# Kernel optimization log

Measured on AMD Instinct MI355X. Metric: run time of the kernel, lower is better.

Reference implementation:

```python
import jax, jax.numpy as jnp
import numpy as np
from jax import lax

B, C, H, W = 2, 256, 64, 64
CI = C // 2           # inter_channels = 128
CH = CI // 2          # key/query channels = 64
EPS = 1e-5


def conv1x1(x, w, b):
    # x: [B,C,H,W], w: [O,C], b: [O]
    return jnp.einsum('oc,bchw->bohw', w, x) + b[None, :, None, None]


def bn(x, g, be, m, v):
    inv = (g / jnp.sqrt(v + EPS))[None, :, None, None]
    return (x - m[None, :, None, None]) * inv + be[None, :, None, None]


def setup_inputs() -> dict:
    key = jax.random.key(0)
    ks = jax.random.split(key, 40)
    r = lambda i, shape, sc=0.05: jax.random.normal(ks[i], shape, dtype=jnp.float32) * sc
    u = lambda i, shape: jax.random.uniform(ks[i], shape, dtype=jnp.float32, minval=0.5, maxval=1.5)
    return {
        'q': jax.random.normal(ks[0], (B, C, H, W), dtype=jnp.float32),
        's': jax.random.normal(ks[1], (B, C, H, W), dtype=jnp.float32),
        'scale': jnp.full((1,), 0.3, dtype=jnp.float32),
        'w_v': r(2, (CI, C)), 'b_v': r(3, (CI,)),
        'w_k1': r(4, (CH, C)), 'b_k1': r(5, (CH,)),
        'w_q1': r(6, (CH, C)), 'b_q1': r(7, (CH,)),
        'w_k2': r(8, (CH, C)), 'b_k2': r(9, (CH,)),
        'w_q2': r(10, (CH, C)), 'b_q2': r(11, (CH,)),
        'w_ts': r(12, (CI, C)), 'b_ts': r(13, (CI,)),
        'g_ts': u(14, (CI,)), 'be_ts': r(15, (CI,)), 'm_ts': r(16, (CI,)), 'v_ts': u(17, (CI,)),
        'w_tq': r(18, (CI, C)), 'b_tq': r(19, (CI,)),
        'g_tq': u(20, (CI,)), 'be_tq': r(21, (CI,)), 'm_tq': r(22, (CI,)), 'v_tq': u(23, (CI,)),
        'w_cat': r(24, (CI, 2 * CI, 3, 3)),
        'g_cat': u(25, (CI,)), 'be_cat': r(26, (CI,)), 'm_cat': r(27, (CI,)), 'v_cat': u(28, (CI,)),
    }


def reference(q, s, scale, w_v, b_v, w_k1, b_k1, w_q1, b_q1, w_k2, b_k2, w_q2, b_q2,
              w_ts, b_ts, g_ts, be_ts, m_ts, v_ts,
              w_tq, b_tq, g_tq, be_tq, m_tq, v_tq,
              w_cat, g_cat, be_cat, m_cat, v_cat):
    b_, _, h, w = q.shape
    n = h * w
    # values: [B, N, CI]
    v_q = conv1x1(q, w_v, b_v).reshape(b_, CI, n).transpose(0, 2, 1)
    v_s = conv1x1(s, w_v, b_v).reshape(b_, CI, n).transpose(0, 2, 1)
    # concatenated keys/queries: [B, CI, N]
    k_x = jnp.concatenate([conv1x1(q, w_k1, b_k1), conv1x1(s, w_k2, b_k2)], axis=1).reshape(b_, CI, n)
    q_x = jnp.concatenate([conv1x1(q, w_q1, b_q1), conv1x1(s, w_q2, b_q2)], axis=1).reshape(b_, CI, n)
    # affinity: [B, N, N]
    A_s = jnp.einsum('bcn,bcm->bnm', k_x, q_x)
    attn_s = jax.nn.softmax(A_s, axis=-1)
    attn_q = jax.nn.softmax(jnp.transpose(A_s, (0, 2, 1)), axis=-1)
    # p_s: [B, N, CI] -> [B, CI, H, W]
    p_s = jnp.einsum('bnm,bmc->bnc', attn_s, v_s).transpose(0, 2, 1).reshape(b_, CI, h, w)
    s_t = bn(conv1x1(s, w_ts, b_ts), g_ts, be_ts, m_ts, v_ts)
    q_t = bn(conv1x1(q, w_tq, b_tq), g_tq, be_tq, m_tq, v_tq)
    E_s = scale[0] * p_s + s_t
    q_s_ = jnp.einsum('bnm,bmc->bnc', attn_q, v_q).transpose(0, 2, 1).reshape(b_, CI, h, w)
    E_q = scale[0] * q_s_ + q_t
    cat = jnp.concatenate([E_q, E_s], axis=1)
    conv = lax.conv_general_dilated(cat, w_cat, (1, 1), 'SAME',
                                    dimension_numbers=('NCHW', 'OIHW', 'NCHW'))
    cpam = jax.nn.relu(bn(conv, g_cat, be_cat, m_cat, v_cat))
    return (cpam, E_q, E_s)
```

## Files before the change

### kernel.cpp

```cpp
#include <hip/hip_runtime.h>
#include <hip/hip_bf16.h>

#define NPIX 4096
#define NCH  256
#define CI   128
#define EPS  1e-5f
#define SOFF 20.0f

typedef unsigned short u16;
typedef __attribute__((ext_vector_type(8))) short short8;
typedef __attribute__((ext_vector_type(4))) float f32x4;
typedef __attribute__((ext_vector_type(16))) float f32x16;

__device__ __forceinline__ float bfu2f(u16 u) {
    union { unsigned int i; float f; } x; x.i = ((unsigned int)u) << 16; return x.f;
}
__device__ __forceinline__ u16 f2bfu(float f) {
    union { float ff; unsigned int i; } x; x.ff = f;
    unsigned int r = x.i + 0x7FFFu + ((x.i >> 16) & 1u);
    return (u16)(r >> 16);
}

__device__ __forceinline__ void gload16(const u16* g, u16* l) {
    __builtin_amdgcn_global_load_lds(
        (const __attribute__((address_space(1))) unsigned int*)g,
        (__attribute__((address_space(3))) unsigned int*)l,
        16, 0, 0);
}

__global__ __launch_bounds__(256) void prep_kernel(
    const float* __restrict__ w_v,
    const float* __restrict__ w_k1, const float* __restrict__ w_q1,
    const float* __restrict__ w_k2, const float* __restrict__ w_q2,
    const float* __restrict__ w_ts, const float* __restrict__ w_tq,
    u16* __restrict__ Wbf,
    const float* __restrict__ w_cat, u16* __restrict__ wT)
{
    const int bx = blockIdx.x;
    if (bx < 768) {
        int idx = bx * 256 + threadIdx.x;
        int src = idx / 98304;
        int r   = idx - src * 98304;
        int o   = r >> 8, c = r & 255;
        float v;
        if (o < 128)      v = w_v[(size_t)o * 256 + c];
        else if (o < 192) v = (src ? w_k2 : w_k1)[(size_t)(o - 128) * 256 + c];
        else if (o < 256) v = (src ? w_q2 : w_q1)[(size_t)(o - 192) * 256 + c];
        else              v = (src ? w_ts : w_tq)[(size_t)(o - 256) * 256 + c];
        Wbf[idx] = f2bfu(v);
    } else {
        int co = bx - 768;
        const float* srcb = w_cat + (size_t)co * 2304;
        u16* dstb = wT + (size_t)co * 2304;
        for (int t = threadIdx.x; t < 2304; t += 256) {
            int ic = t / 9, tap = t - ic * 9;
            dstb[tap * 256 + ic] = f2bfu(srcb[t]);
        }
    }
}

__global__ __launch_bounds__(256) void proj2_kernel(
    const float* __restrict__ xq, const float* __restrict__ xs,
    const u16* __restrict__ Wbf,
    const float* __restrict__ b_v,
    const float* __restrict__ b_k1, const float* __restrict__ b_q1,
    const float* __restrict__ b_k2, const float* __restrict__ b_q2,
    const float* __restrict__ b_ts, const float* __restrict__ g_ts,
    const float* __restrict__ be_ts, const float* __restrict__ m_ts,
    const float* __restrict__ v_ts,
    const float* __restrict__ b_tq, const float* __restrict__ g_tq,
    const float* __restrict__ be_tq, const float* __restrict__ m_tq,
    const float* __restrict__ v_tq,
    u16* __restrict__ kT, u16* __restrict__ qT,
    u16* __restrict__ vq, u16* __restrict__ vs,
    u16* __restrict__ tq, u16* __restrict__ ts)
{
    __shared__ u16 Xs[64 * 264];
    __shared__ u16 KQ[64 * 136];

    const int tid  = threadIdx.x;
    const int lane = tid & 63;
    const int wid  = tid >> 6;
    const int l16  = lane & 15;
    const int quad = lane >> 4;

    const int n0  = blockIdx.x * 64;
    const int bz  = blockIdx.z;
    const int b   = bz >> 1, src = bz & 1;

    const float* xg = (src ? xs : xq) + (size_t)b * NCH * NPIX + n0;
    #pragma unroll
    for (int k0 = 0; k0 < 64; k0 += 16) {
        float v[16];
        #pragma unroll
        for (int k = 0; k < 16; ++k) {
            int idx = tid + (k0 + k) * 256;
            int c = idx >> 6, n = idx & 63;
            v[k] = xg[(size_t)c * NPIX + n];
        }
        #pragma unroll
        for (int k = 0; k < 16; ++k) {
            int idx = tid + (k0 + k) * 256;
            int c = idx >> 6, n = idx & 63;
            Xs[n * 264 + c] = f2bfu(v[k]);
        }
    }
    __syncthreads();

    const u16* W = Wbf + (size_t)src * 384 * 256;
    const int o0w = wid * 96;
    const float* bk = src ? b_k2 : b_k1;
    const float* bq = src ? b_q2 : b_q1;
    const float* bt = src ? b_ts : b_tq;

    f32x4 acc[24];
    #pragma unroll
    for (int ot = 0; ot < 6; ++ot) {
        int ob = o0w + ot * 16 + quad * 4;
        const float* bp;
        if (ob < 128)      bp = b_v + ob;
        else if (ob < 192) bp = bk + (ob - 128);
        else if (ob < 256) bp = bq + (ob - 192);
        else               bp = bt + (ob - 256);
        float4 b4 = *(const float4*)bp;
        f32x4 iv = (f32x4){b4.x, b4.y, b4.z, b4.w};
        #pragma unroll
        for (int pt = 0; pt < 4; ++pt) acc[ot * 4 + pt] = iv;
    }

    #pragma unroll
    for (int kc = 0; kc < 8; ++kc) {
        short8 bfr[4];
        #pragma unroll
        for (int pt = 0; pt < 4; ++pt)
            bfr[pt] = *(const short8*)&Xs[(pt * 16 + l16) * 264 + kc * 32 + quad * 8];
        #pragma unroll
        for (int ot = 0; ot < 6; ++ot) {
            short8 a = *(const short8*)&W[(size_t)(o0w + ot * 16 + l16) * 256 + kc * 32 + quad * 8];
            #pragma unroll
            for (int pt = 0; pt < 4; ++pt)
                acc[ot * 4 + pt] = __builtin_amdgcn_mfma_f32_16x16x32_bf16(a, bfr[pt], acc[ot * 4 + pt], 0, 0, 0);
        }
    }

    #pragma unroll
    for (int ot = 0; ot < 6; ++ot) {
        int ob = o0w + ot * 16;
        #pragma unroll
        for (int pt = 0; pt < 4; ++pt) {
            int px = pt * 16 + l16;
            f32x4 v4 = acc[ot * 4 + pt];
            if (ob < 128) {
                u16* dst = src ? vs : vq;
                #pragma unroll
                for (int r = 0; r < 4; ++r)
                    dst[((size_t)b * CI + ob + quad * 4 + r) * NPIX + n0 + px] = f2bfu(v4[r]);
            } else if (ob < 256) {
                int colb = (ob < 192) ? (ob - 128) : (64 + ob - 192);
                #pragma unroll
                for (int r = 0; r < 4; ++r)
                    KQ[px * 136 + colb + quad * 4 + r] = f2bfu(v4[r]);
            } else {
                const float* g  = src ? g_ts  : g_tq;
                const float* be = src ? be_ts : be_tq;
                const float* mm = src ? m_ts  : m_tq;
                const float* vv = src ? v_ts  : v_tq;
                u16* dst = src ? ts : tq;
                #pragma unroll
                for (int r = 0; r < 4; ++r) {
                    int oc = ob - 256 + quad * 4 + r;
                    float inv = g[oc] * rsqrtf(vv[oc] + EPS);
                    dst[((size_t)b * CI + oc) * NPIX + n0 + px] =
                        f2bfu((v4[r] - mm[oc]) * inv + be[oc]);
                }
            }
        }
    }
    __syncthreads();

    const int chb = src ? 64 : 0;
    #pragma unroll
    for (int u = 0; u < 4; ++u) {
        int idx = tid + u * 256;
        int px = idx >> 4, oct = idx & 15;
        uint4 val = *(const uint4*)&KQ[px * 136 + oct * 8];
        if (oct < 8)
            *(uint4*)&kT[((size_t)b * NPIX + n0 + px) * CI + chb + oct * 8] = val;
        else
            *(uint4*)&qT[((size_t)b * NPIX + n0 + px) * CI + chb + (oct - 8) * 8] = val;
    }
}

#define AKS_OFF 0
#define AVT_OFF 8192
#define ASMEM_U16 16384

__global__ __launch_bounds__(128) void attn_kernel(
    const u16* __restrict__ kT, const u16* __restrict__ qT,
    const u16* __restrict__ vq, const u16* __restrict__ vs,
    u16* __restrict__ Opart, float* __restrict__ Lpart, int nseg)
{
    __shared__ __align__(16) u16 smem[ASMEM_U16];

    const int tid  = threadIdx.x;
    const int lane = tid & 63;
    const int qh   = tid >> 6;
    const int l32  = lane & 31;
    const int h    = lane >> 5;

    const int nt = blockIdx.x;
    const int n0 = nt * 64;
    const int at = blockIdx.y;
    const int z  = blockIdx.z;
    const int b  = z / nseg;
    const int seg = z - b * nseg;

    const u16* Qg = at ? qT : kT;
    const u16* Kg = at ? kT : qT;
    const u16* Vg = at ? vq : vs;

    short8 qf[8];
    {
        const u16* Qb = Qg + ((size_t)b * NPIX + n0 + qh * 32 + l32) * CI;
        #pragma unroll
        for (int kc = 0; kc < 8; ++kc)
            qf[kc] = *(const short8*)&Qb[kc * 16 + h * 8];
    }

    f32x16 o[4];
    #pragma unroll
    for (int ct = 0; ct < 4; ++ct)
        #pragma unroll
        for (int r = 0; r < 16; ++r) o[ct][r] = 0.f;
    float L = 0.f;

    const u16* KgB = Kg + (size_t)b * NPIX * CI;
    const u16* VgB = Vg + (size_t)b * CI * NPIX;

    const int mt0 = seg * (128 / nseg);
    const int mt1 = mt0 + (128 / nseg);

    const int fv = (l32 >> 1) & 3;

    #define ISSUE_TILE(buf, m0_)                                              \
    {                                                                         \
        u16* kb_ = smem + AKS_OFF + (buf) * 4096;                             \
        u16* vb_ = smem + AVT_OFF + (buf) * 4096;                             \
        _Pragma("unroll")                                                     \
        for (int k = 0; k < 4; ++k) {                                         \
            int sb  = k * 128 + qh * 64;                                      \
            int idx = sb + lane;                                              \
            int row = idx >> 4, p = idx & 15;                                 \
            int pg = p ^ (row & 15);                                          \
            gload16(KgB + (size_t)((m0_) + row) * CI + pg * 8, kb_ + sb * 8); \
        }                                                                     \
        _Pragma("unroll")                                                     \
        for (int k = 0; k < 4; ++k) {                                         \
            int sb  = k * 128 + qh * 64;                                      \
            int idx = sb + lane;                                              \
            int c = idx >> 2, p = idx & 3;                                    \
            int pg = p ^ ((c >> 1) & 3);                                      \
            gload16(VgB + (size_t)c * NPIX + (m0_) + pg * 8, vb_ + sb * 8);   \
        }                                                                     \
    }

    int cur = 0;
    ISSUE_TILE(0, mt0 * 32);

    for (int mt = mt0; mt < mt1; ++mt) {
        __syncthreads();
        if (mt + 1 < mt1) ISSUE_TILE(1 - cur, (mt + 1) * 32);

        const u16* Ks = smem + AKS_OFF + cur * 4096;
        const u16* Vt = smem + AVT_OFF + cur * 4096;

        f32x16 c;
        #pragma unroll
        for (int r = 0; r < 16; ++r) c[r] = 0.f;
        __builtin_amdgcn_s_setprio(1);
        #pragma unroll
        for (int kc = 0; kc < 8; ++kc) {
            short8 kf = *(const short8*)&Ks[l32 * 128 + (((kc * 2 + h) ^ (l32 & 15)) * 8)];
            c = __builtin_amdgcn_mfma_f32_32x32x16_bf16(kf, qf[kc], c, 0, 0, 0);
        }
        __builtin_amdgcn_s_setprio(0);

        unsigned int pk[8];
        float Lsum = 0.f;
        #pragma unroll
        for (int t = 0; t < 8; ++t) {
            float p0 = __expf(c[2 * t]     - SOFF);
            float p1 = __expf(c[2 * t + 1] - SOFF);
            Lsum += p0 + p1;
            asm("v_cvt_pk_bf16_f32 %0, %1, %2" : "=v"(pk[t]) : "v"(p0), "v"(p1));
        }
        Lsum += __shfl_xor(Lsum, 32);
        L += Lsum;

        unsigned int pw0 = __shfl_xor(pk[0], 32), pw1 = __shfl_xor(pk[1], 32);
        unsigned int pw2 = __shfl_xor(pk[2], 32), pw3 = __shfl_xor(pk[3], 32);
        unsigned int pw4 = __shfl_xor(pk[4], 32), pw5 = __shfl_xor(pk[5], 32);
        unsigned int pw6 = __shfl_xor(pk[6], 32), pw7 = __shfl_xor(pk[7], 32);
        union { unsigned int u[4]; short8 s8; } a0, a1;
        a0.u[0] = h ? pw2 : pk[0];
        a0.u[1] = h ? pw3 : pk[1];
        a0.u[2] = h ? pk[2] : pw0;
        a0.u[3] = h ? pk[3] : pw1;
        a1.u[0] = h ? pw6 : pk[4];
        a1.u[1] = h ? pw7 : pk[5];
        a1.u[2] = h ? pk[6] : pw4;
        a1.u[3] = h ? pk[7] : pw5;

        __builtin_amdgcn_s_setprio(1);
        #pragma unroll
        for (int ct = 0; ct < 4; ++ct) {
            int ci = ct * 32 + l32;
            short8 b0 = *(const short8*)&Vt[ci * 32 + (((    h) ^ fv) * 8)];
            o[ct] = __builtin_amdgcn_mfma_f32_32x32x16_bf16(a0.s8, b0, o[ct], 0, 0, 0);
            short8 b1 = *(const short8*)&Vt[ci * 32 + (((2 + h) ^ fv) * 8)];
            o[ct] = __builtin_amdgcn_mfma_f32_32x32x16_bf16(a1.s8, b1, o[ct], 0, 0, 0);
        }
        __builtin_amdgcn_s_setprio(0);
        cur ^= 1;
    }

    const size_t tile = (((size_t)(at * 2 + b) * 64 + nt) * nseg + seg);
    u16* Ob = Opart + tile * 8192;
    #pragma unroll
    for (int r = 0; r < 16; ++r) {
        int row = qh * 32 + (r & 3) + 8 * (r >> 2) + 4 * h;
        #pragma unroll
        for (int ct = 0; ct < 4; ++ct)
            Ob[row * 128 + ct * 32 + l32] = f2bfu(o[ct][r]);
    }
    if (h == 0)
        Lpart[tile * 64 + qh * 32 + l32] = L;
    #undef ISSUE_TILE
}

__global__ __launch_bounds__(256) void attn_combine_kernel(
    const u16* __restrict__ Opart, const float* __restrict__ Lpart,
    const u16* __restrict__ tq, const u16* __restrict__ ts,
    const float* __restrict__ scale_p,
    float* __restrict__ out, u16* __restrict__ Ebf, int nseg)
{
    __shared__ float Of[128 * 68];
    __shared__ float invL[64];

    const int tid = threadIdx.x;
    const int nt = blockIdx.x;
    const int n0 = nt * 64;
    const int at = blockIdx.y;
    const int b  = blockIdx.z;

    const u16* Tg = at ? tq : ts;
    float* outE   = out + (size_t)(at ? 1 : 2) * 1048576;
    const int ch0 = at ? 0 : 128;
    const size_t tbase = ((size_t)(at * 2 + b) * 64 + nt) * nseg;

    if (tid < 64) {
        float Lg = 0.f;
        for (int s = 0; s < nseg; ++s) Lg += Lpart[(tbase + s) * 64 + tid];
        invL[tid] = 1.f / Lg;
    }
    __syncthreads();

    #pragma unroll
    for (int k = 0; k < 4; ++k) {
        int idx = tid + k * 256;
        int row = idx >> 4, oct = idx & 15;
        float m[8] = {0.f, 0.f, 0.f, 0.f, 0.f, 0.f, 0.f, 0.f};
        for (int s = 0; s < nseg; ++s) {
            union { uint4 v; u16 u[8]; } pk;
            pk.v = *(const uint4*)&Opart[(tbase + s) * 8192 + row * 128 + oct * 8];
            #pragma unroll
            for (int j = 0; j < 8; ++j) m[j] += bfu2f(pk.u[j]);
        }
        float w = invL[row];
        #pragma unroll
        for (int j = 0; j < 8; ++j)
            Of[(oct * 8 + j) * 68 + row] = m[j] * w;
    }
    __syncthreads();

    float scale = *scale_p;
    const u16* Tb = Tg + (size_t)b * CI * NPIX + n0;
    float* Ob = outE + (size_t)b * CI * NPIX + n0;
    for (int idx = tid; idx < 128 * 64; idx += 256) {
        int c = idx >> 6, r = idx & 63;
        float v = scale * Of[c * 68 + r] + bfu2f(Tb[(size_t)c * NPIX + r]);
        Ob[(size_t)c * NPIX + r] = v;
        Ebf[((size_t)b * NPIX + n0 + r) * NCH + ch0 + c] = f2bfu(v);
    }
}

#define CXT_STR 40

__global__ __launch_bounds__(256) void conv_kernel(
    const u16* __restrict__ Ebf,
    const u16* __restrict__ wT,
    const float* __restrict__ g_cat, const float* __restrict__ be_cat,
    const float* __restrict__ m_cat, const float* __restrict__ v_cat,
    float* __restrict__ out)
{
    __shared__ u16 XtW[4][3 * 34 * CXT_STR];

    const int tid  = threadIdx.x;
    const int lane = tid & 63;
    const int wid  = tid >> 6;
    const int l16  = lane & 15;
    const int quad = lane >> 4;

    const int h    = blockIdx.x;
    const int coff = blockIdx.y * 32;
    const int b    = blockIdx.z;

    const int cot = wid >> 1;
    const int pxt = (wid & 1) * 2;
    const int gc0 = pxt * 16 - 1;

    f32x4 acc[2];
    #pragma unroll
    for (int j = 0; j < 2; ++j) acc[j] = (f32x4){0.f, 0.f, 0.f, 0.f};

    const u16* Eb = Ebf + (size_t)b * NPIX * NCH;
    u16* Xw = &XtW[wid][0];
    const int cobase = coff + cot * 16 + l16;

    for (int icc = 0; icc < 8; ++icc) {
        const int ic0 = icc * 32;

        short8 wfrag[9];
        #pragma unroll
        for (int tap = 0; tap < 9; ++tap)
            wfrag[tap] = *(const short8*)&wT[((size_t)cobase * 9 + tap) * 256 + ic0 + quad * 8];

        for (int u = lane; u < 408; u += 64) {
            int part = u & 3, xe = u >> 2;
            int dh = xe / 34, x = xe - dh * 34;
            int gr = h + dh - 1, gc = gc0 + x;
            uint4 val = make_uint4(0u, 0u, 0u, 0u);
            if ((unsigned)gr < 64u && (unsigned)gc < 64u)
                val = *(const uint4*)&Eb[((size_t)gr * 64 + gc) * NCH + ic0 + part * 8];
            *(uint4*)&Xw[(dh * 34 + x) * CXT_STR + part * 8] = val;
        }

        #pragma unroll
        for (int tap = 0; tap < 9; ++tap) {
            const int dh = tap / 3, dw = tap % 3;
            short8 bf[2];
            #pragma unroll
            for (int j = 0; j < 2; ++j) {
                int x = j * 16 + l16 + dw;
                bf[j] = *(const short8*)&Xw[(dh * 34 + x) * CXT_STR + quad * 8];
            }
            #pragma unroll
            for (int j = 0; j < 2; ++j)
                acc[j] = __builtin_amdgcn_mfma_f32_16x16x32_bf16(wfrag[tap], bf[j], acc[j], 0, 0, 0);
        }
    }

    #pragma unroll
    for (int r = 0; r < 4; ++r) {
        int co = coff + cot * 16 + quad * 4 + r;
        float inv = g_cat[co] * rsqrtf(v_cat[co] + EPS);
        float mm  = m_cat[co];
        float be  = be_cat[co];
        #pragma unroll
        for (int j = 0; j < 2; ++j) {
            int wcol = (pxt + j) * 16 + l16;
            float v = (acc[j][r] - mm) * inv + be;
            out[((size_t)b * CI + co) * NPIX + h * 64 + wcol] = fmaxf(v, 0.f);
        }
    }
}

extern "C" void kernel_launch(void* const* d_in, const int* in_sizes, int n_in,
                              void* d_out, int out_size, void* d_ws, size_t ws_size,
                              hipStream_t stream)
{
    const float* q     = (const float*)d_in[0];
    const float* s     = (const float*)d_in[1];
    const float* scale = (const float*)d_in[2];
    const float* w_v   = (const float*)d_in[3];
    const float* b_v   = (const float*)d_in[4];
    const float* w_k1  = (const float*)d_in[5];
    const float* b_k1  = (const float*)d_in[6];
    const float* w_q1  = (const float*)d_in[7];
    const float* b_q1  = (const float*)d_in[8];
    const float* w_k2  = (const float*)d_in[9];
    const float* b_k2  = (const float*)d_in[10];
    const float* w_q2  = (const float*)d_in[11];
    const float* b_q2  = (const float*)d_in[12];
    const float* w_ts  = (const float*)d_in[13];
    const float* b_ts  = (const float*)d_in[14];
    const float* g_ts  = (const float*)d_in[15];
    const float* be_ts = (const float*)d_in[16];
    const float* m_ts  = (const float*)d_in[17];
    const float* v_ts  = (const float*)d_in[18];
    const float* w_tq  = (const float*)d_in[19];
    const float* b_tq  = (const float*)d_in[20];
    const float* g_tq  = (const float*)d_in[21];
    const float* be_tq = (const float*)d_in[22];
    const float* m_tq  = (const float*)d_in[23];
    const float* v_tq  = (const float*)d_in[24];
    const float* w_cat = (const float*)d_in[25];
    const float* g_cat = (const float*)d_in[26];
    const float* be_cat= (const float*)d_in[27];
    const float* m_cat = (const float*)d_in[28];
    const float* v_cat = (const float*)d_in[29];

    float* out = (float*)d_out;
    u16* ws = (u16*)d_ws;
    const size_t SZ = (size_t)2 * CI * NPIX;
    u16* kT  = ws;
    u16* qT  = kT + SZ;
    u16* vq  = qT + SZ;
    u16* vs  = vq + SZ;
    u16* tq  = vs + SZ;
    u16* ts  = tq + SZ;
    u16* Wbf = ts + SZ;
    u16* B   = Wbf + 196608;
    u16* Ebf = B;
    u16* wTc = B + 2097152;
    u16* Opart = wTc + 294912;

    const size_t fixed_u16 = 6 * SZ + 196608 + 2097152 + 294912;
    int nseg = 1;
    {
        size_t need4 = (fixed_u16 + (size_t)4 * 2097152) * 2 + (size_t)4 * 131072;
        size_t need2 = (fixed_u16 + (size_t)2 * 2097152) * 2 + (size_t)2 * 131072;
        if (ws_size >= need4)      nseg = 4;
        else if (ws_size >= need2) nseg = 2;
    }
    float* Lpart = (float*)(Opart + (size_t)nseg * 256 * 8192);

    dim3 blk(256);
    hipLaunchKernelGGL(prep_kernel, dim3(896), blk, 0, stream,
                       w_v, w_k1, w_q1, w_k2, w_q2, w_ts, w_tq, Wbf, w_cat, wTc);
    hipLaunchKernelGGL(proj2_kernel, dim3(64, 1, 4), blk, 0, stream,
                       q, s, Wbf, b_v, b_k1, b_q1, b_k2, b_q2,
                       b_ts, g_ts, be_ts, m_ts, v_ts,
                       b_tq, g_tq, be_tq, m_tq, v_tq,
                       kT, qT, vq, vs, tq, ts);
    hipLaunchKernelGGL(attn_kernel, dim3(64, 2, 2 * nseg), dim3(128), 0, stream,
                       kT, qT, vq, vs, Opart, Lpart, nseg);
    hipLaunchKernelGGL(attn_combine_kernel, dim3(64, 2, 2), blk, 0, stream,
                       Opart, Lpart, tq, ts, scale, out, Ebf, nseg);
    hipLaunchKernelGGL(conv_kernel, dim3(64, 4, 2), blk, 0, stream,
                       Ebf, wTc, g_cat, be_cat, m_cat, v_cat, out);
}
```

Baseline: 245.4 us.

## Load attention K fragments directly to registers and use permlane32 swaps

```diff
diff --git a/kernel.cpp b/kernel.cpp
--- a/kernel.cpp
+++ b/kernel.cpp
@@ -191,9 +191,7 @@
     }
 }
 
-#define AKS_OFF 0
-#define AVT_OFF 8192
-#define ASMEM_U16 16384
+#define ASMEM_U16 8192
 
 __global__ __launch_bounds__(128) void attn_kernel(
     const u16* __restrict__ kT, const u16* __restrict__ qT,
@@ -242,87 +240,92 @@
 
     const int fv = (l32 >> 1) & 3;
 
-    #define ISSUE_TILE(buf, m0_)                                              \
+    const int pg = (tid & 3) ^ ((tid >> 3) & 3);
+    const u16* Vsrc = VgB + (size_t)(tid >> 2) * NPIX + pg * 8;
+
+    const u16* Kp = KgB + ((size_t)(mt0 * 32) + l32) * CI + h * 8;
+
+    short8 kfA[8], kfB[8];
+    #pragma unroll
+    for (int kc = 0; kc < 8; ++kc) kfA[kc] = *(const short8*)&Kp[kc * 16];
+
+    #define ISSUE_V(BUF2, M0_)                                                \
+    {   u16* vb_ = smem + (BUF2) * 4096;                                      \
+        _Pragma("unroll")                                                     \
+        for (int k = 0; k < 4; ++k)                                           \
+            gload16(Vsrc + (size_t)k * 32 * NPIX + (M0_),                     \
+                    vb_ + (k * 128 + qh * 64) * 8);                           \
+    }
+
+    ISSUE_V(0, mt0 * 32);
+
+    #define STEP(KFC, KFN, BUF, MT)                                           \
     {                                                                         \
-        u16* kb_ = smem + AKS_OFF + (buf) * 4096;                             \
-        u16* vb_ = smem + AVT_OFF + (buf) * 4096;                             \
+               \
+        f32x16 c;                                                             \
+        _Pragma("unroll") for (int r = 0; r < 16; ++r) c[r] = 0.f;            \
+        __builtin_amdgcn_s_setprio(1);                                        \
         _Pragma("unroll")                                                     \
-        for (int k = 0; k < 4; ++k) {                                         \
-            int sb  = k * 128 + qh * 64;                                      \
-            int idx = sb + lane;                                              \
-            int row = idx >> 4, p = idx & 15;                                 \
-            int pg = p ^ (row & 15);                                          \
-            gload16(KgB + (size_t)((m0_) + row) * CI + pg * 8, kb_ + sb * 8); \
+        for (int kc = 0; kc < 8; ++kc)                                        \
+            c = __builtin_amdgcn_mfma_f32_32x32x16_bf16(KFC[kc], qf[kc], c, 0, 0, 0); \
+        __builtin_amdgcn_s_setprio(0);                                        \
+               \
+        unsigned int pk[8];                                                   \
+        float Lsum = 0.f;                                                     \
+        _Pragma("unroll")                                                     \
+        for (int t = 0; t < 8; ++t) {                                         \
+            float p0 = __expf(c[2 * t]     - SOFF);                           \
+            float p1 = __expf(c[2 * t + 1] - SOFF);                           \
+            Lsum += p0 + p1;                                                  \
+            asm("v_cvt_pk_bf16_f32 %0, %1, %2" : "=v"(pk[t]) : "v"(p0), "v"(p1)); \
         }                                                                     \
+        {                                                                     \
+            union { float f; unsigned int u; } lu; lu.f = Lsum;               \
+            unsigned int la = lu.u, lb = lu.u;                                \
+            asm("v_permlane32_swap_b32 %0, %1" : "+v"(la), "+v"(lb));         \
+            union { unsigned int u; float f; } lp; lp.u = h ? la : lb;        \
+            L += Lsum + lp.f;                                                 \
+        }                                                                     \
+          \
+        unsigned int x0 = pk[0], x2 = pk[2];                                  \
+        asm("v_permlane32_swap_b32 %0, %1" : "+v"(x0), "+v"(x2));             \
+        unsigned int x1 = pk[1], x3 = pk[3];                                  \
+        asm("v_permlane32_swap_b32 %0, %1" : "+v"(x1), "+v"(x3));             \
+        unsigned int x4 = pk[4], x6 = pk[6];                                  \
+        asm("v_permlane32_swap_b32 %0, %1" : "+v"(x4), "+v"(x6));             \
+        unsigned int x5 = pk[5], x7 = pk[7];                                  \
+        asm("v_permlane32_swap_b32 %0, %1" : "+v"(x5), "+v"(x7));             \
+        union { unsigned int u[4]; short8 s8; } a0, a1;                       \
+        a0.u[0] = x0; a0.u[1] = x1; a0.u[2] = x2; a0.u[3] = x3;               \
+        a1.u[0] = x4; a1.u[1] = x5; a1.u[2] = x6; a1.u[3] = x7;               \
+        __syncthreads();           \
+        if ((MT) + 1 < mt1) {                                                 \
+            ISSUE_V(1 - (BUF), ((MT) + 1) * 32);                              \
+            Kp += 32 * CI;                                                    \
+            _Pragma("unroll")                                                 \
+            for (int kc = 0; kc < 8; ++kc)                                    \
+                KFN[kc] = *(const short8*)&Kp[kc * 16];                       \
+        }                                                                     \
+                  \
+        const u16* Vt = smem + (BUF) * 4096;                                  \
+        __builtin_amdgcn_s_setprio(1);                                        \
         _Pragma("unroll")                                                     \
-        for (int k = 0; k < 4; ++k) {                                         \
-            int sb  = k * 128 + qh * 64;                                      \
-            int idx = sb + lane;                                              \
-            int c = idx >> 2, p = idx & 3;                                    \
-            int pg = p ^ ((c >> 1) & 3);                                      \
-            gload16(VgB + (size_t)c * NPIX + (m0_) + pg * 8, vb_ + sb * 8);   \
+        for (int ct = 0; ct < 4; ++ct) {                                      \
+            int ci = ct * 32 + l32;                                           \
+            short8 b0 = *(const short8*)&Vt[ci * 32 + ((h ^ fv) * 8)];        \
+            o[ct] = __builtin_amdgcn_mfma_f32_32x32x16_bf16(a0.s8, b0, o[ct], 0, 0, 0); \
+            short8 b1 = *(const short8*)&Vt[ci * 32 + (((2 + h) ^ fv) * 8)];  \
+            o[ct] = __builtin_amdgcn_mfma_f32_32x32x16_bf16(a1.s8, b1, o[ct], 0, 0, 0); \
         }                                                                     \
-    }
-
-    int cur = 0;
-    ISSUE_TILE(0, mt0 * 32);
-
-    for (int mt = mt0; mt < mt1; ++mt) {
-        __syncthreads();
-        if (mt + 1 < mt1) ISSUE_TILE(1 - cur, (mt + 1) * 32);
-
-        const u16* Ks = smem + AKS_OFF + cur * 4096;
-        const u16* Vt = smem + AVT_OFF + cur * 4096;
-
-        f32x16 c;
-        #pragma unroll
-        for (int r = 0; r < 16; ++r) c[r] = 0.f;
-        __builtin_amdgcn_s_setprio(1);
-        #pragma unroll
-        for (int kc = 0; kc < 8; ++kc) {
-            short8 kf = *(const short8*)&Ks[l32 * 128 + (((kc * 2 + h) ^ (l32 & 15)) * 8)];
-            c = __builtin_amdgcn_mfma_f32_32x32x16_bf16(kf, qf[kc], c, 0, 0, 0);
-        }
-        __builtin_amdgcn_s_setprio(0);
-
-        unsigned int pk[8];
-        float Lsum = 0.f;
-        #pragma unroll
-        for (int t = 0; t < 8; ++t) {
-            float p0 = __expf(c[2 * t]     - SOFF);
-            float p1 = __expf(c[2 * t + 1] - SOFF);
-            Lsum += p0 + p1;
-            asm("v_cvt_pk_bf16_f32 %0, %1, %2" : "=v"(pk[t]) : "v"(p0), "v"(p1));
-        }
-        Lsum += __shfl_xor(Lsum, 32);
-        L += Lsum;
-
-        unsigned int pw0 = __shfl_xor(pk[0], 32), pw1 = __shfl_xor(pk[1], 32);
-        unsigned int pw2 = __shfl_xor(pk[2], 32), pw3 = __shfl_xor(pk[3], 32);
-        unsigned int pw4 = __shfl_xor(pk[4], 32), pw5 = __shfl_xor(pk[5], 32);
-        unsigned int pw6 = __shfl_xor(pk[6], 32), pw7 = __shfl_xor(pk[7], 32);
-        union { unsigned int u[4]; short8 s8; } a0, a1;
-        a0.u[0] = h ? pw2 : pk[0];
-        a0.u[1] = h ? pw3 : pk[1];
-        a0.u[2] = h ? pk[2] : pw0;
-        a0.u[3] = h ? pk[3] : pw1;
-        a1.u[0] = h ? pw6 : pk[4];
-        a1.u[1] = h ? pw7 : pk[5];
-        a1.u[2] = h ? pk[6] : pw4;
-        a1.u[3] = h ? pk[7] : pw5;
-
-        __builtin_amdgcn_s_setprio(1);
-        #pragma unroll
-        for (int ct = 0; ct < 4; ++ct) {
-            int ci = ct * 32 + l32;
-            short8 b0 = *(const short8*)&Vt[ci * 32 + (((    h) ^ fv) * 8)];
-            o[ct] = __builtin_amdgcn_mfma_f32_32x32x16_bf16(a0.s8, b0, o[ct], 0, 0, 0);
-            short8 b1 = *(const short8*)&Vt[ci * 32 + (((2 + h) ^ fv) * 8)];
-            o[ct] = __builtin_amdgcn_mfma_f32_32x32x16_bf16(a1.s8, b1, o[ct], 0, 0, 0);
-        }
-        __builtin_amdgcn_s_setprio(0);
-        cur ^= 1;
-    }
+        __builtin_amdgcn_s_setprio(0);                                        \
+    }
+
+    for (int mt = mt0; mt < mt1; mt += 2) {
+        STEP(kfA, kfB, 0, mt)
+        STEP(kfB, kfA, 1, mt + 1)
+    }
+    #undef STEP
+    #undef ISSUE_V
 
     const size_t tile = (((size_t)(at * 2 + b) * 64 + nt) * nseg + seg);
     u16* Ob = Opart + tile * 8192;
@@ -335,7 +338,6 @@
     }
     if (h == 0)
         Lpart[tile * 64 + qh * 32 + l32] = L;
-    #undef ISSUE_TILE
 }
 
 __global__ __launch_bounds__(256) void attn_combine_kernel(
```

After: 265.5 us. 1.08x slower.

## Load V fragments directly from global, use permlane32 swaps, allow eight key segments

Applied to the files above, without the earlier changes.

```diff
diff --git a/kernel.cpp b/kernel.cpp
--- a/kernel.cpp
+++ b/kernel.cpp
@@ -191,11 +191,9 @@
     }
 }
 
-#define AKS_OFF 0
-#define AVT_OFF 8192
-#define ASMEM_U16 16384
-
-__global__ __launch_bounds__(128) void attn_kernel(
+#define ASMEM_U16 8192
+
+__global__ __launch_bounds__(128, 3) void attn_kernel(
     const u16* __restrict__ kT, const u16* __restrict__ qT,
     const u16* __restrict__ vq, const u16* __restrict__ vs,
     u16* __restrict__ Opart, float* __restrict__ Lpart, int nseg)
@@ -237,15 +235,15 @@
     const u16* KgB = Kg + (size_t)b * NPIX * CI;
     const u16* VgB = Vg + (size_t)b * CI * NPIX;
 
-    const int mt0 = seg * (128 / nseg);
-    const int mt1 = mt0 + (128 / nseg);
-
-    const int fv = (l32 >> 1) & 3;
-
-    #define ISSUE_TILE(buf, m0_)                                              \
+    const int mtn = 128 / nseg;
+    const int mt0 = seg * mtn;
+    const int mt1 = mt0 + mtn;
+
+    const u16* Vb = VgB + (size_t)l32 * NPIX + h * 8;
+
+    #define ISSUE_K(buf, m0_)                                                 \
     {                                                                         \
-        u16* kb_ = smem + AKS_OFF + (buf) * 4096;                             \
-        u16* vb_ = smem + AVT_OFF + (buf) * 4096;                             \
+        u16* kb_ = smem + (buf) * 4096;                                       \
         _Pragma("unroll")                                                     \
         for (int k = 0; k < 4; ++k) {                                         \
             int sb  = k * 128 + qh * 64;                                      \
@@ -254,25 +252,26 @@
             int pg = p ^ (row & 15);                                          \
             gload16(KgB + (size_t)((m0_) + row) * CI + pg * 8, kb_ + sb * 8); \
         }                                                                     \
-        _Pragma("unroll")                                                     \
-        for (int k = 0; k < 4; ++k) {                                         \
-            int sb  = k * 128 + qh * 64;                                      \
-            int idx = sb + lane;                                              \
-            int c = idx >> 2, p = idx & 3;                                    \
-            int pg = p ^ ((c >> 1) & 3);                                      \
-            gload16(VgB + (size_t)c * NPIX + (m0_) + pg * 8, vb_ + sb * 8);   \
-        }                                                                     \
     }
 
     int cur = 0;
-    ISSUE_TILE(0, mt0 * 32);
+    ISSUE_K(0, mt0 * 32);
 
     for (int mt = mt0; mt < mt1; ++mt) {
+        const int m0 = mt * 32;
         __syncthreads();
-        if (mt + 1 < mt1) ISSUE_TILE(1 - cur, (mt + 1) * 32);
-
-        const u16* Ks = smem + AKS_OFF + cur * 4096;
-        const u16* Vt = smem + AVT_OFF + cur * 4096;
+
+        short8 vf[8];
+        #pragma unroll
+        for (int ct = 0; ct < 4; ++ct) {
+            vf[2 * ct]     = *(const short8*)&Vb[(size_t)(ct * 32) * NPIX + m0];
+            vf[2 * ct + 1] = *(const short8*)&Vb[(size_t)(ct * 32) * NPIX + m0 + 16];
+        }
+        __builtin_amdgcn_sched_barrier(0);
+
+        if (mt + 1 < mt1) ISSUE_K(1 - cur, (mt + 1) * 32);
+
+        const u16* Ks = smem + cur * 4096;
 
         f32x16 c;
         #pragma unroll
@@ -294,35 +293,36 @@
             Lsum += p0 + p1;
             asm("v_cvt_pk_bf16_f32 %0, %1, %2" : "=v"(pk[t]) : "v"(p0), "v"(p1));
         }
-        Lsum += __shfl_xor(Lsum, 32);
-        L += Lsum;
-
-        unsigned int pw0 = __shfl_xor(pk[0], 32), pw1 = __shfl_xor(pk[1], 32);
-        unsigned int pw2 = __shfl_xor(pk[2], 32), pw3 = __shfl_xor(pk[3], 32);
-        unsigned int pw4 = __shfl_xor(pk[4], 32), pw5 = __shfl_xor(pk[5], 32);
-        unsigned int pw6 = __shfl_xor(pk[6], 32), pw7 = __shfl_xor(pk[7], 32);
+        {
+            union { float f; unsigned int u; } lu; lu.f = Lsum;
+            unsigned int la = lu.u, lb = lu.u;
+            asm("v_permlane32_swap_b32 %0, %1" : "+v"(la), "+v"(lb));
+            union { unsigned int u; float f; } lp; lp.u = h ? la : lb;
+            L += Lsum + lp.f;
+        }
+
+        unsigned int x0 = pk[0], x2 = pk[2];
+        asm("v_permlane32_swap_b32 %0, %1" : "+v"(x0), "+v"(x2));
+        unsigned int x1 = pk[1], x3 = pk[3];
+        asm("v_permlane32_swap_b32 %0, %1" : "+v"(x1), "+v"(x3));
+        unsigned int x4 = pk[4], x6 = pk[6];
+        asm("v_permlane32_swap_b32 %0, %1" : "+v"(x4), "+v"(x6));
+        unsigned int x5 = pk[5], x7 = pk[7];
+        asm("v_permlane32_swap_b32 %0, %1" : "+v"(x5), "+v"(x7));
         union { unsigned int u[4]; short8 s8; } a0, a1;
-        a0.u[0] = h ? pw2 : pk[0];
-        a0.u[1] = h ? pw3 : pk[1];
-        a0.u[2] = h ? pk[2] : pw0;
-        a0.u[3] = h ? pk[3] : pw1;
-        a1.u[0] = h ? pw6 : pk[4];
-        a1.u[1] = h ? pw7 : pk[5];
-        a1.u[2] = h ? pk[6] : pw4;
-        a1.u[3] = h ? pk[7] : pw5;
+        a0.u[0] = x0; a0.u[1] = x1; a0.u[2] = x2; a0.u[3] = x3;
+        a1.u[0] = x4; a1.u[1] = x5; a1.u[2] = x6; a1.u[3] = x7;
 
         __builtin_amdgcn_s_setprio(1);
         #pragma unroll
         for (int ct = 0; ct < 4; ++ct) {
-            int ci = ct * 32 + l32;
-            short8 b0 = *(const short8*)&Vt[ci * 32 + (((    h) ^ fv) * 8)];
-            o[ct] = __builtin_amdgcn_mfma_f32_32x32x16_bf16(a0.s8, b0, o[ct], 0, 0, 0);
-            short8 b1 = *(const short8*)&Vt[ci * 32 + (((2 + h) ^ fv) * 8)];
-            o[ct] = __builtin_amdgcn_mfma_f32_32x32x16_bf16(a1.s8, b1, o[ct], 0, 0, 0);
+            o[ct] = __builtin_amdgcn_mfma_f32_32x32x16_bf16(a0.s8, vf[2 * ct],     o[ct], 0, 0, 0);
+            o[ct] = __builtin_amdgcn_mfma_f32_32x32x16_bf16(a1.s8, vf[2 * ct + 1], o[ct], 0, 0, 0);
         }
         __builtin_amdgcn_s_setprio(0);
         cur ^= 1;
     }
+    #undef ISSUE_K
 
     const size_t tile = (((size_t)(at * 2 + b) * 64 + nt) * nseg + seg);
     u16* Ob = Opart + tile * 8192;
@@ -335,7 +335,6 @@
     }
     if (h == 0)
         Lpart[tile * 64 + qh * 32 + l32] = L;
-    #undef ISSUE_TILE
 }
 
 __global__ __launch_bounds__(256) void attn_combine_kernel(
@@ -528,9 +527,11 @@
     const size_t fixed_u16 = 6 * SZ + 196608 + 2097152 + 294912;
     int nseg = 1;
     {
+        size_t need8 = (fixed_u16 + (size_t)8 * 2097152) * 2 + (size_t)8 * 131072;
         size_t need4 = (fixed_u16 + (size_t)4 * 2097152) * 2 + (size_t)4 * 131072;
         size_t need2 = (fixed_u16 + (size_t)2 * 2097152) * 2 + (size_t)2 * 131072;
-        if (ws_size >= need4)      nseg = 4;
+        if (ws_size >= need8)      nseg = 8;
+        else if (ws_size >= need4) nseg = 4;
         else if (ws_size >= need2) nseg = 2;
     }
     float* Lpart = (float*)(Opart + (size_t)nseg * 256 * 8192);
```

Measured after the change: 327.0 us. 33.3% more time.
